# Kernel tuning notes

Hardware: AMD Instinct MI355X
Metric: run time of the kernel (lower is better)

Reference implementation:

```python
import jax, jax.numpy as jnp
import numpy as np

# Dims: B agents, C=64 channels (hardcoded in module), HxW BEV map,
# L=3 residual VQ stages, S=4 segments, M=256 codewords, D=C/S=16.
B, C, H, W = 4, 64, 256, 256
L, S, M = 3, 4, 256
D = C // S


def setup_inputs() -> dict:
    key = jax.random.key(0)
    ks = jax.random.split(key, 13)
    def w(k, shape, scale=0.125):
        return jax.random.normal(k, shape, dtype=jnp.float32) * scale
    return {
        "heter_feature_2d": jax.random.normal(ks[0], (B, C, H, W), dtype=jnp.float32),
        # Stacked per-stage Linear(64,64) weights for the six UMGM heads.
        "W_enc": w(ks[1], (L, C, C)), "b_enc": jnp.zeros((L, C), jnp.float32),  # latentStageEncoder
        "W_qh":  w(ks[2], (L, C, C)), "b_qh":  jnp.zeros((L, C), jnp.float32),  # quantizationHead
        "W_lh":  w(ks[3], (L, C, C)), "b_lh":  jnp.zeros((L, C), jnp.float32),  # latentHead
        "W_dq":  w(ks[4], (L, C, C)), "b_dq":  jnp.zeros((L, C), jnp.float32),  # dequantizationHead
        "W_rh":  w(ks[5], (L, C, C)), "b_rh":  jnp.zeros((L, C), jnp.float32),  # restoreHead
        # Per-stage, per-segment codebooks: [L, S, M, D]
        "codebooks": w(ks[6], (L, S, M, D), 1.0),
    }


def reference(heter_feature_2d, W_enc, b_enc, W_qh, b_qh, W_lh, b_lh,
              W_dq, b_dq, W_rh, b_rh, codebooks):
    Bq, Cq, Hq, Wq = heter_feature_2d.shape
    Lq, Sq, Mq, Dq = codebooks.shape
    # permute(0,2,3,1).view(-1, C)
    x = heter_feature_2d.transpose(0, 2, 3, 1).reshape(-1, Cq)  # [N, C]
    N = x.shape[0]

    residual = x
    restored = jnp.zeros_like(x)
    loss = jnp.float32(0.0)
    commit_w = jnp.float32(0.25)
    for i in range(Lq):  # fixed small number of residual-VQ stages
        z = residual @ W_enc[i] + b_enc[i]                       # [N, C]
        q = (z @ W_qh[i] + b_qh[i]).reshape(N, Sq, Dq)           # [N, S, D]
        cb = codebooks[i]                                        # [S, M, D]
        # squared L2 distances to every codeword, per segment: [N, S, M]
        dist = ((q * q).sum(-1)[..., None]
                - 2.0 * jnp.einsum('nsd,smd->nsm', q, cb)
                + (cb * cb).sum(-1)[None])
        idx = jnp.argmin(dist, axis=-1)                          # [N, S] int
        hard = cb[jnp.arange(Sq)[None, :], idx]                  # gather: [N, S, D]
        # codebook + commitment loss
        loss = loss + jnp.mean((jax.lax.stop_gradient(q) - hard) ** 2) \
                    + commit_w * jnp.mean((q - jax.lax.stop_gradient(hard)) ** 2)
        # straight-through quantization
        quant = (q + jax.lax.stop_gradient(hard - q)).reshape(N, Cq)
        deq = quant @ W_dq[i] + b_dq[i]
        restored = restored + deq @ W_rh[i] + b_rh[i]
        residual = (z @ W_lh[i] + b_lh[i]) - deq                 # next-stage residual

    out = restored.reshape(Bq, Hq, Wq, Cq).transpose(0, 3, 1, 2)  # back to [B, C, H, W]
    return out, loss
```

## Files before the change

kernel.cpp:

```cpp
#include <hip/hip_runtime.h>

#define HW 65536
#define STRIDE 68

typedef float          f32x4  __attribute__((ext_vector_type(4)));
typedef __bf16         bf16x8 __attribute__((ext_vector_type(8)));
typedef unsigned short u16x8  __attribute__((ext_vector_type(8)));


__device__ __forceinline__ f32x4 mfma16(bf16x8 a, bf16x8 b, f32x4 c) {
    return __builtin_amdgcn_mfma_f32_16x16x32_bf16(a, b, c, 0, 0, 0);
}

struct AFrag { bf16x8 a1[2], a2[2], a3[2]; };

__device__ __forceinline__ void split3_8(const float* f, bf16x8* v1, bf16x8* v2, bf16x8* v3) {
    u16x8 a, b, c;
    #pragma unroll
    for (int i = 0; i < 8; ++i) {
        const float    x  = f[i];
        const unsigned u1 = __float_as_uint(x) & 0xFFFF0000u;
        const float    r1 = x - __uint_as_float(u1);
        const unsigned u2 = __float_as_uint(r1) & 0xFFFF0000u;
        const float    r2 = r1 - __uint_as_float(u2);
        const unsigned u3 = __float_as_uint(r2) & 0xFFFF0000u;
        a[i] = (unsigned short)(u1 >> 16);
        b[i] = (unsigned short)(u2 >> 16);
        c[i] = (unsigned short)(u3 >> 16);
    }
    union { u16x8 u; bf16x8 b; } cv;
    cv.u = a; *v1 = cv.b;
    cv.u = b; *v2 = cv.b;
    cv.u = c; *v3 = cv.b;
}

__device__ __forceinline__ AFrag load_afrag(const float* __restrict__ buf, int rbase, int lane) {
    const int r  = rbase + (lane & 15);
    const int k0 = (lane >> 4) * 8;
    const float* p = buf + r * STRIDE + k0;
    float f[16];
    *(float4*)(f + 0)  = *(const float4*)(p + 0);
    *(float4*)(f + 4)  = *(const float4*)(p + 4);
    *(float4*)(f + 8)  = *(const float4*)(p + 32);
    *(float4*)(f + 12) = *(const float4*)(p + 36);
    AFrag A;
    split3_8(f,     &A.a1[0], &A.a2[0], &A.a3[0]);
    split3_8(f + 8, &A.a1[1], &A.a2[1], &A.a3[1]);
    return A;
}

template<int MODE>
__device__ __forceinline__ void mm64(float* __restrict__ dst, const float* __restrict__ src,
                                     const __bf16* __restrict__ wt, const float* __restrict__ bias,
                                     f32x4* __restrict__ sav, int lane, int w)
{
    const AFrag A = load_afrag(src, w * 16, lane);
    const int lc = lane & 15;
    const int kg = (lane >> 4) * 8;
    const int rg = (lane >> 4) * 4;
    #pragma unroll
    for (int ct = 0; ct < 4; ++ct) {
        const int col = ct * 16 + lc;
        const __bf16* wp = wt + col * 64 + kg;
        const bf16x8 b10 = *(const bf16x8*)(wp);
        const bf16x8 b11 = *(const bf16x8*)(wp + 32);
        const bf16x8 b20 = *(const bf16x8*)(wp + 4096);
        const bf16x8 b21 = *(const bf16x8*)(wp + 4096 + 32);
        const bf16x8 b30 = *(const bf16x8*)(wp + 8192);
        const bf16x8 b31 = *(const bf16x8*)(wp + 8192 + 32);
        const float bv = bias[col];
        f32x4 acc;
        if (MODE == 2) { acc = sav[ct]; acc.x += bv; acc.y += bv; acc.z += bv; acc.w += bv; }
        else           { acc.x = bv; acc.y = bv; acc.z = bv; acc.w = bv; }
        acc = mfma16(A.a1[0], b10, acc); acc = mfma16(A.a1[1], b11, acc);
        acc = mfma16(A.a2[0], b10, acc); acc = mfma16(A.a2[1], b11, acc);
        acc = mfma16(A.a3[0], b10, acc); acc = mfma16(A.a3[1], b11, acc);
        acc = mfma16(A.a1[0], b20, acc); acc = mfma16(A.a1[1], b21, acc);
        acc = mfma16(A.a2[0], b20, acc); acc = mfma16(A.a2[1], b21, acc);
        acc = mfma16(A.a1[0], b30, acc); acc = mfma16(A.a1[1], b31, acc);
        if (MODE == 2) { sav[ct] = acc; continue; }
        if (MODE == 1) sav[ct] = acc;
        if (MODE == 3) { const f32x4 d = sav[ct]; acc.x -= d.x; acc.y -= d.y; acc.z -= d.z; acc.w -= d.w; }
        #pragma unroll
        for (int j = 0; j < 4; ++j)
            dst[(w * 16 + rg + j) * STRIDE + col] = acc[j];
    }
}

__global__ __launch_bounds__(256)
void hpp_prep(const float* __restrict__ W_enc, const float* __restrict__ W_qh,
              const float* __restrict__ W_dq,  const float* __restrict__ W_rh,
              const float* __restrict__ W_lh,
              __bf16* __restrict__ ws)
{
    const int i = blockIdx.x * 256 + threadIdx.x;
    if (i < 61440) {
        const int m = i >> 12, e = i & 4095;
        const int t = m / 3, L = m - t * 3;
        const int c = e >> 6, k = e & 63;
        const float* W = (t == 0) ? W_enc : (t == 1) ? W_qh : (t == 2) ? W_dq
                                        : (t == 3) ? W_rh : W_lh;
        const float    fv = W[L * 4096 + k * 64 + c];
        const unsigned u1 = __float_as_uint(fv) & 0xFFFF0000u;
        const float    r1 = fv - __uint_as_float(u1);
        const unsigned u2 = __float_as_uint(r1) & 0xFFFF0000u;
        const float    r2 = r1 - __uint_as_float(u2);
        const unsigned u3 = __float_as_uint(r2) & 0xFFFF0000u;
        unsigned short* wp = (unsigned short*)(ws + m * 12288 + c * 64 + k);
        wp[0]    = (unsigned short)(u1 >> 16);
        wp[4096] = (unsigned short)(u2 >> 16);
        wp[8192] = (unsigned short)(u3 >> 16);
    }
}

__global__ __launch_bounds__(256, 2)
void hpp_fused(const float* __restrict__ x,
               const float* __restrict__ b_enc, const float* __restrict__ b_qh,
               const float* __restrict__ b_lh,  const float* __restrict__ b_dq,
               const float* __restrict__ b_rh,
               const float* __restrict__ cbk,   const __bf16* __restrict__ ws,
               float* __restrict__ out, float* __restrict__ loss_out)
{
    __shared__ __align__(16) float buf0[64 * STRIDE];
    __shared__ __align__(16) float buf1[64 * STRIDE];
    __shared__ __align__(16) float buf2[64 * STRIDE];
    __shared__ float cc[256];
    __shared__ float red_d[256];
    __shared__ int   red_i[256];
    __shared__ float wred[4];

    const int t   = threadIdx.x;
    const int n0  = blockIdx.x * 64;
    const int b   = n0 >> 16;
    const int hw0 = n0 & (HW - 1);
    const size_t base = (size_t)b * 64 * HW + hw0;

    float* rb = buf0;
    float* zb = buf1;
    float* qb = buf2;

    for (int i = 0; i < 16; ++i) {
        const int e = t + 256 * i;
        const int c = e >> 6, r = e & 63;
        rb[r * STRIDE + c] = x[base + (size_t)c * HW + r];
    }

    const int lane = t & 63;
    const int w    = t >> 6;
    const int lc   = lane & 15;
    const int g2   = lane >> 4;

    f32x4 restored[4] = {};
    f32x4 deqf[4];
    float loss_acc = 0.f;

    __syncthreads();

    for (int L = 0; L < 3; ++L) {
        const __bf16* wtE = ws + (0 * 3 + L) * 12288;
        const __bf16* wtQ = ws + (1 * 3 + L) * 12288;
        const __bf16* wtD = ws + (2 * 3 + L) * 12288;
        const __bf16* wtR = ws + (3 * 3 + L) * 12288;
        const __bf16* wtL = ws + (4 * 3 + L) * 12288;

        mm64<0>(zb, rb, wtE, b_enc + L * 64, nullptr, lane, w);
        __syncthreads();
        mm64<0>(qb, zb, wtQ, b_qh + L * 64, nullptr, lane, w);

        for (int s = 0; s < 4; ++s) {
            __syncthreads();
            const float4* __restrict__ cbs4 = (const float4*)(cbk + (size_t)(L * 4 + s) * 4096);
            float4* __restrict__ rb4 = (float4*)rb;
            #pragma unroll
            for (int i = 0; i < 4; ++i)
                rb4[t + 256 * i] = cbs4[t + 256 * i];
            __syncthreads();
            {
                float s0 = 0, s1 = 0, s2 = 0, s3 = 0;
                const float* cp = rb + t * 16;
                #pragma unroll
                for (int d4 = 0; d4 < 4; ++d4) {
                    const float4 v = *(const float4*)(cp + 4 * d4);
                    s0 = fmaf(v.x, v.x, s0); s1 = fmaf(v.y, v.y, s1);
                    s2 = fmaf(v.z, v.z, s2); s3 = fmaf(v.w, v.w, s3);
                }
                cc[t] = (s0 + s1) + (s2 + s3);
            }
            __syncthreads();
            {
                const int row = t & 63, qt = t >> 6;
                float qv[16];
                const float* qp = qb + row * STRIDE + s * 16;
                #pragma unroll
                for (int d4 = 0; d4 < 4; ++d4) {
                    const float4 v = *(const float4*)(qp + 4 * d4);
                    qv[4 * d4 + 0] = v.x; qv[4 * d4 + 1] = v.y;
                    qv[4 * d4 + 2] = v.z; qv[4 * d4 + 3] = v.w;
                }
                float qq = 0.f;
                #pragma unroll
                for (int d = 0; d < 16; ++d) qq = fmaf(qv[d], qv[d], qq);
                float best = 3.4e38f; int bi = 0;
                #pragma unroll 2
                for (int mi = 0; mi < 64; ++mi) {
                    const int m = qt * 64 + mi;
                    const float* cp = rb + m * 16;
                    float d0 = 0, d1 = 0, d2 = 0, d3 = 0;
                    #pragma unroll
                    for (int d4 = 0; d4 < 4; ++d4) {
                        const float4 v = *(const float4*)(cp + 4 * d4);
                        d0 = fmaf(qv[4 * d4 + 0], v.x, d0);
                        d1 = fmaf(qv[4 * d4 + 1], v.y, d1);
                        d2 = fmaf(qv[4 * d4 + 2], v.z, d2);
                        d3 = fmaf(qv[4 * d4 + 3], v.w, d3);
                    }
                    const float dot  = (d0 + d1) + (d2 + d3);
                    const float dist = qq - 2.0f * dot + cc[m];
                    if (dist < best) { best = dist; bi = m; }
                }
                red_d[qt * 64 + row] = best;
                red_i[qt * 64 + row] = bi;
            }
            __syncthreads();
            if (t < 64) {
                const int row = t;
                float best = red_d[row]; int bi = red_i[row];
                #pragma unroll
                for (int qt = 1; qt < 4; ++qt) {
                    const float dv = red_d[qt * 64 + row];
                    if (dv < best) { best = dv; bi = red_i[qt * 64 + row]; }
                }
                float* qp = qb + row * STRIDE + s * 16;
                const float* hp = rb + bi * 16;
                float lsum = 0.f;
                #pragma unroll
                for (int d = 0; d < 16; ++d) {
                    const float qvv = qp[d];
                    const float hv  = hp[d];
                    const float e   = qvv - hv;
                    lsum = fmaf(e, e, lsum);
                    qp[d] = hv;
                }
                loss_acc += lsum;
            }
        }
        __syncthreads();

        mm64<1>(rb, qb, wtD, b_dq + L * 64, deqf, lane, w);
        __syncthreads();
        mm64<2>(nullptr, rb, wtR, b_rh + L * 64, restored, lane, w);
        if (L < 2)
            mm64<3>(qb, zb, wtL, b_lh + L * 64, deqf, lane, w);
        __syncthreads();
        float* tmp = rb; rb = qb; qb = tmp;
    }

    #pragma unroll
    for (int off = 32; off > 0; off >>= 1) loss_acc += __shfl_down(loss_acc, off, 64);
    if (lane == 0) wred[w] = loss_acc;

    {
        const int rg = g2 * 4;
        #pragma unroll
        for (int ct = 0; ct < 4; ++ct)
            #pragma unroll
            for (int j = 0; j < 4; ++j)
                zb[(w * 16 + rg + j) * STRIDE + ct * 16 + lc] = restored[ct][j];
    }
    __syncthreads();
    for (int i = 0; i < 16; ++i) {
        const int e = t + 256 * i;
        const int c = e >> 6, r = e & 63;
        out[base + (size_t)c * HW + r] = zb[r * STRIDE + c];
    }
    if (t == 0) {
        const float tot = (wred[0] + wred[1]) + (wred[2] + wred[3]);
        atomicAdd(loss_out, tot * (1.25f / 16777216.0f));
    }
}

extern "C" void kernel_launch(void* const* d_in, const int* in_sizes, int n_in,
                              void* d_out, int out_size, void* d_ws, size_t ws_size,
                              hipStream_t stream) {
    const float* x     = (const float*)d_in[0];
    const float* W_enc = (const float*)d_in[1];
    const float* b_enc = (const float*)d_in[2];
    const float* W_qh  = (const float*)d_in[3];
    const float* b_qh  = (const float*)d_in[4];
    const float* W_lh  = (const float*)d_in[5];
    const float* b_lh  = (const float*)d_in[6];
    const float* W_dq  = (const float*)d_in[7];
    const float* b_dq  = (const float*)d_in[8];
    const float* W_rh  = (const float*)d_in[9];
    const float* b_rh  = (const float*)d_in[10];
    const float* cbk   = (const float*)d_in[11];

    float* out      = (float*)d_out;
    float* loss_out = out + (out_size - 1);

    __bf16* ws = (__bf16*)d_ws;

    hipMemsetAsync(loss_out, 0, sizeof(float), stream);
    hpp_prep<<<dim3(240), dim3(256), 0, stream>>>(W_enc, W_qh, W_dq, W_rh, W_lh, ws);
    hpp_fused<<<dim3(4096), dim3(256), 0, stream>>>(
        x, b_enc, b_qh, b_lh, b_dq, b_rh, cbk, ws, out, loss_out);
}
```

Before: 1.275 ms.

## Compute VQ codeword distances with split-bf16 MFMA and precomputed codebook norms

Moves the per-segment nearest-codeword search from scalar FP32 dot products over an LDS-staged codebook to MFMA. The codebook is pre-split into three bf16 parts and its squared norms are precomputed in the prep kernel. Each wave handles one segment, reduces the argmin with cross-lane shuffles, and computes the loss from the min distance plus |q|^2. It also swaps several __syncthreads for per-wave lgkmcnt waits. This removes the codebook copies into LDS and most barriers, but the split-bf16 distances and dropped barriers risk argmin ties or precision mismatches and cross-wave LDS races.

```diff
diff --git a/kernel.cpp b/kernel.cpp
--- a/kernel.cpp
+++ b/kernel.cpp
@@ -7,6 +7,10 @@
 typedef __bf16         bf16x8 __attribute__((ext_vector_type(8)));
 typedef unsigned short u16x8  __attribute__((ext_vector_type(8)));
 
+#define LGKM0() asm volatile("s_waitcnt lgkmcnt(0)" ::: "memory")
+
+#define WS_CB 184320
+#define WS_CC 331776
 
 __device__ __forceinline__ f32x4 mfma16(bf16x8 a, bf16x8 b, f32x4 c) {
     return __builtin_amdgcn_mfma_f32_16x16x32_bf16(a, b, c, 0, 0, 0);
@@ -90,7 +94,7 @@
 __global__ __launch_bounds__(256)
 void hpp_prep(const float* __restrict__ W_enc, const float* __restrict__ W_qh,
               const float* __restrict__ W_dq,  const float* __restrict__ W_rh,
-              const float* __restrict__ W_lh,
+              const float* __restrict__ W_lh,  const float* __restrict__ cbk,
               __bf16* __restrict__ ws)
 {
     const int i = blockIdx.x * 256 + threadIdx.x;
@@ -110,6 +114,25 @@
         wp[0]    = (unsigned short)(u1 >> 16);
         wp[4096] = (unsigned short)(u2 >> 16);
         wp[8192] = (unsigned short)(u3 >> 16);
+    } else if (i < 110592) {
+        const int j = i - 61440;
+        const float    fv = cbk[j];
+        const unsigned u1 = __float_as_uint(fv) & 0xFFFF0000u;
+        const float    r1 = fv - __uint_as_float(u1);
+        const unsigned u2 = __float_as_uint(r1) & 0xFFFF0000u;
+        const float    r2 = r1 - __uint_as_float(u2);
+        const unsigned u3 = __float_as_uint(r2) & 0xFFFF0000u;
+        unsigned short* cp = (unsigned short*)(ws + WS_CB + j);
+        cp[0]     = (unsigned short)(u1 >> 16);
+        cp[49152] = (unsigned short)(u2 >> 16);
+        cp[98304] = (unsigned short)(u3 >> 16);
+    } else if (i < 113664) {
+        const int j = i - 110592;
+        const float* cp = cbk + (size_t)j * 16;
+        float s0 = 0.f;
+        #pragma unroll
+        for (int d = 0; d < 16; ++d) s0 = fmaf(cp[d], cp[d], s0);
+        ((float*)(ws + WS_CC))[j] = s0;
     }
 }
 
@@ -124,7 +147,6 @@
     __shared__ __align__(16) float buf0[64 * STRIDE];
     __shared__ __align__(16) float buf1[64 * STRIDE];
     __shared__ __align__(16) float buf2[64 * STRIDE];
-    __shared__ float cc[256];
     __shared__ float red_d[256];
     __shared__ int   red_i[256];
     __shared__ float wred[4];
@@ -153,6 +175,8 @@
     f32x4 restored[4] = {};
     f32x4 deqf[4];
     float loss_acc = 0.f;
+
+    const float* ccp_all = (const float*)(ws + WS_CC);
 
     __syncthreads();
 
@@ -164,94 +188,114 @@
         const __bf16* wtL = ws + (4 * 3 + L) * 12288;
 
         mm64<0>(zb, rb, wtE, b_enc + L * 64, nullptr, lane, w);
+        LGKM0();
+        mm64<0>(qb, zb, wtQ, b_qh + L * 64, nullptr, lane, w);
         __syncthreads();
-        mm64<0>(qb, zb, wtQ, b_qh + L * 64, nullptr, lane, w);
-
-        for (int s = 0; s < 4; ++s) {
-            __syncthreads();
-            const float4* __restrict__ cbs4 = (const float4*)(cbk + (size_t)(L * 4 + s) * 4096);
-            float4* __restrict__ rb4 = (float4*)rb;
-            #pragma unroll
-            for (int i = 0; i < 4; ++i)
-                rb4[t + 256 * i] = cbs4[t + 256 * i];
-            __syncthreads();
-            {
-                float s0 = 0, s1 = 0, s2 = 0, s3 = 0;
-                const float* cp = rb + t * 16;
+
+        {
+            const int ls   = L * 4 + w;
+            const int dsel = (g2 & 1) * 8;
+            const __bf16* cbL = ws + WS_CB + ls * 4096;
+            const __bf16* bp1 = cbL + (g2 < 2 ? 0 : 1) * 49152;
+            const __bf16* bp2 = cbL + (g2 < 2 ? 1 : 0) * 49152;
+            const __bf16* bp3 = cbL + (g2 < 2 ? 2 : 0) * 49152;
+            const float*  ccp = ccp_all + ls * 256;
+
+            for (int rt = 0; rt < 4; ++rt) {
+                const int row = rt * 16 + lc;
+                const float* qp = qb + row * STRIDE + w * 16 + dsel;
+                float f[8];
+                *(float4*)(f + 0) = *(const float4*)(qp + 0);
+                *(float4*)(f + 4) = *(const float4*)(qp + 4);
+                bf16x8 q1, q2, q3;
+                {
+                    u16x8 ua, ub, uc;
+                    #pragma unroll
+                    for (int i2 = 0; i2 < 8; ++i2) {
+                        const float    v  = -2.0f * f[i2];
+                        const unsigned u1 = __float_as_uint(v) & 0xFFFF0000u;
+                        const float    r1 = v - __uint_as_float(u1);
+                        const unsigned u2 = __float_as_uint(r1) & 0xFFFF0000u;
+                        const float    r2 = r1 - __uint_as_float(u2);
+                        const unsigned u3 = __float_as_uint(r2) & 0xFFFF0000u;
+                        ua[i2] = (unsigned short)(u1 >> 16);
+                        ub[i2] = (unsigned short)(u2 >> 16);
+                        uc[i2] = (unsigned short)(u3 >> 16);
+                    }
+                    union { u16x8 u; bf16x8 b; } cv;
+                    cv.u = ua; q1 = cv.b;
+                    cv.u = ub; q2 = cv.b;
+                    cv.u = uc; q3 = cv.b;
+                }
+                const bf16x8 a12 = (g2 < 2) ? q1 : q2;
+                const bf16x8 a13 = (g2 < 2) ? q1 : q3;
+
+                float bd[4]; int bi[4];
                 #pragma unroll
-                for (int d4 = 0; d4 < 4; ++d4) {
-                    const float4 v = *(const float4*)(cp + 4 * d4);
-                    s0 = fmaf(v.x, v.x, s0); s1 = fmaf(v.y, v.y, s1);
-                    s2 = fmaf(v.z, v.z, s2); s3 = fmaf(v.w, v.w, s3);
+                for (int j = 0; j < 4; ++j) { bd[j] = 3.4e38f; bi[j] = 0; }
+
+                #pragma unroll 4
+                for (int ct = 0; ct < 16; ++ct) {
+                    const int code = ct * 16 + lc;
+                    const int co   = code * 16 + dsel;
+                    const bf16x8 B1 = *(const bf16x8*)(bp1 + co);
+                    const bf16x8 B2 = *(const bf16x8*)(bp2 + co);
+                    const bf16x8 B3 = *(const bf16x8*)(bp3 + co);
+                    const float ccv = ccp[code];
+                    f32x4 acc = {ccv, ccv, ccv, ccv};
+                    acc = mfma16(a12, B1, acc);
+                    acc = mfma16(a12, B2, acc);
+                    acc = mfma16(a13, B3, acc);
+                    #pragma unroll
+                    for (int j = 0; j < 4; ++j)
+                        if (acc[j] < bd[j]) { bd[j] = acc[j]; bi[j] = code; }
                 }
-                cc[t] = (s0 + s1) + (s2 + s3);
-            }
-            __syncthreads();
-            {
-                const int row = t & 63, qt = t >> 6;
-                float qv[16];
-                const float* qp = qb + row * STRIDE + s * 16;
                 #pragma unroll
-                for (int d4 = 0; d4 < 4; ++d4) {
-                    const float4 v = *(const float4*)(qp + 4 * d4);
-                    qv[4 * d4 + 0] = v.x; qv[4 * d4 + 1] = v.y;
-                    qv[4 * d4 + 2] = v.z; qv[4 * d4 + 3] = v.w;
+                for (int j = 0; j < 4; ++j) {
+                    float d = bd[j]; int ix = bi[j];
+                    #pragma unroll
+                    for (int m = 1; m < 16; m <<= 1) {
+                        const float od = __shfl_xor(d, m, 64);
+                        const int   oi = __shfl_xor(ix, m, 64);
+                        if (od < d || (od == d && oi < ix)) { d = od; ix = oi; }
+                    }
+                    if (lc == 0) {
+                        red_d[w * 64 + rt * 16 + g2 * 4 + j] = d;
+                        red_i[w * 64 + rt * 16 + g2 * 4 + j] = ix;
+                    }
                 }
-                float qq = 0.f;
-                #pragma unroll
-                for (int d = 0; d < 16; ++d) qq = fmaf(qv[d], qv[d], qq);
-                float best = 3.4e38f; int bi = 0;
-                #pragma unroll 2
-                for (int mi = 0; mi < 64; ++mi) {
-                    const int m = qt * 64 + mi;
-                    const float* cp = rb + m * 16;
-                    float d0 = 0, d1 = 0, d2 = 0, d3 = 0;
-                    #pragma unroll
-                    for (int d4 = 0; d4 < 4; ++d4) {
-                        const float4 v = *(const float4*)(cp + 4 * d4);
-                        d0 = fmaf(qv[4 * d4 + 0], v.x, d0);
-                        d1 = fmaf(qv[4 * d4 + 1], v.y, d1);
-                        d2 = fmaf(qv[4 * d4 + 2], v.z, d2);
-                        d3 = fmaf(qv[4 * d4 + 3], v.w, d3);
-                    }
-                    const float dot  = (d0 + d1) + (d2 + d3);
-                    const float dist = qq - 2.0f * dot + cc[m];
-                    if (dist < best) { best = dist; bi = m; }
-                }
-                red_d[qt * 64 + row] = best;
-                red_i[qt * 64 + row] = bi;
-            }
-            __syncthreads();
-            if (t < 64) {
-                const int row = t;
-                float best = red_d[row]; int bi = red_i[row];
-                #pragma unroll
-                for (int qt = 1; qt < 4; ++qt) {
-                    const float dv = red_d[qt * 64 + row];
-                    if (dv < best) { best = dv; bi = red_i[qt * 64 + row]; }
-                }
-                float* qp = qb + row * STRIDE + s * 16;
-                const float* hp = rb + bi * 16;
-                float lsum = 0.f;
-                #pragma unroll
-                for (int d = 0; d < 16; ++d) {
-                    const float qvv = qp[d];
-                    const float hv  = hp[d];
-                    const float e   = qvv - hv;
-                    lsum = fmaf(e, e, lsum);
-                    qp[d] = hv;
-                }
-                loss_acc += lsum;
             }
         }
+        LGKM0();
+
+        {
+            const int s = w, row = lane;
+            const float bdv = red_d[s * 64 + row];
+            const int   biv = red_i[s * 64 + row];
+            float* qp = qb + row * STRIDE + s * 16;
+            float qv[16];
+            *(float4*)(qv + 0)  = *(const float4*)(qp + 0);
+            *(float4*)(qv + 4)  = *(const float4*)(qp + 4);
+            *(float4*)(qv + 8)  = *(const float4*)(qp + 8);
+            *(float4*)(qv + 12) = *(const float4*)(qp + 12);
+            float qq = 0.f;
+            #pragma unroll
+            for (int d = 0; d < 16; ++d) qq = fmaf(qv[d], qv[d], qq);
+            loss_acc += bdv + qq;
+            const float* hp = cbk + ((size_t)(L * 4 + s) * 256 + biv) * 16;
+            *(float4*)(qp + 0)  = *(const float4*)(hp + 0);
+            *(float4*)(qp + 4)  = *(const float4*)(hp + 4);
+            *(float4*)(qp + 8)  = *(const float4*)(hp + 8);
+            *(float4*)(qp + 12) = *(const float4*)(hp + 12);
+        }
         __syncthreads();
 
         mm64<1>(rb, qb, wtD, b_dq + L * 64, deqf, lane, w);
-        __syncthreads();
+        LGKM0();
         mm64<2>(nullptr, rb, wtR, b_rh + L * 64, restored, lane, w);
         if (L < 2)
             mm64<3>(qb, zb, wtL, b_lh + L * 64, deqf, lane, w);
-        __syncthreads();
+        LGKM0();
         float* tmp = rb; rb = qb; qb = tmp;
     }
 
@@ -301,7 +345,7 @@
     __bf16* ws = (__bf16*)d_ws;
 
     hipMemsetAsync(loss_out, 0, sizeof(float), stream);
-    hpp_prep<<<dim3(240), dim3(256), 0, stream>>>(W_enc, W_qh, W_dq, W_rh, W_lh, ws);
+    hpp_prep<<<dim3(444), dim3(256), 0, stream>>>(W_enc, W_qh, W_dq, W_rh, W_lh, cbk, ws);
     hpp_fused<<<dim3(4096), dim3(256), 0, stream>>>(
         x, b_enc, b_qh, b_lh, b_dq, b_rh, cbk, ws, out, loss_out);
 }
```

Result: faster. 1.069 ms (-16.2%).
